# Kernel optimization log

Measured on AMD Instinct MI355X. Metric: run time of the kernel, lower is better.

## Reference

```python
import jax, jax.numpy as jnp
import numpy as np

N = 50000
E = 800000
NFEAT = 128
NHID = 128


def _glorot(key, shape):
    fan = shape[0] + shape[-1]
    s = jnp.sqrt(6.0 / fan)
    return jax.random.uniform(key, shape, jnp.float32, -s, s)


def setup_inputs() -> dict:
    key = jax.random.key(0)
    ks = jax.random.split(key, 8)
    x = jax.random.normal(ks[0], (N, NFEAT), jnp.float32)
    edge_index = jax.random.randint(ks[1], (2, E), 0, N, jnp.int64)
    return {
        "x": x,
        "edge_index": edge_index,
        "Wl1": _glorot(ks[2], (NFEAT, NHID)),
        "bl1": jnp.zeros((NHID,), jnp.float32),
        "Wr1": _glorot(ks[3], (NFEAT, NHID)),
        "br1": jnp.zeros((NHID,), jnp.float32),
        "att1": _glorot(ks[4], (NHID,)),
        "b1": jnp.zeros((NHID,), jnp.float32),
        "Wl2": _glorot(ks[5], (NHID, NHID)),
        "bl2": jnp.zeros((NHID,), jnp.float32),
        "Wr2": _glorot(ks[6], (NHID, NHID)),
        "br2": jnp.zeros((NHID,), jnp.float32),
        "att2": _glorot(ks[7], (NHID,)),
        "b2": jnp.zeros((NHID,), jnp.float32),
    }


def gatv2_conv(x, src, dst, Wl, bl, Wr, br, att, bias, neg_slope=0.2):
    # PyG GATv2Conv, heads=1, concat=True, add_self_loops handled by caller.
    xl = x @ Wl + bl                      # [N, H] source transform
    xr = x @ Wr + br                      # [N, H] target transform
    e = jax.nn.leaky_relu(xl[src] + xr[dst], neg_slope) @ att  # [E']
    # segment softmax over incoming edges per destination node
    m = jax.ops.segment_max(e, dst, num_segments=x.shape[0])
    w = jnp.exp(e - m[dst])
    denom = jax.ops.segment_sum(w, dst, num_segments=x.shape[0])
    alpha = w / denom[dst]                # [E']
    out = jax.ops.segment_sum(alpha[:, None] * xl[src], dst,
                              num_segments=x.shape[0])
    return out + bias


def reference(x, edge_index, Wl1, bl1, Wr1, br1, att1, b1,
              Wl2, bl2, Wr2, br2, att2, b2):
    n = x.shape[0]
    loop = jnp.arange(n, dtype=edge_index.dtype)
    src = jnp.concatenate([edge_index[0], loop])  # add self loops (PyG default)
    dst = jnp.concatenate([edge_index[1], loop])
    h = gatv2_conv(x, src, dst, Wl1, bl1, Wr1, br1, att1, b1)
    h = jax.nn.leaky_relu(h, 0.01)  # F.leaky_relu default slope
    out = gatv2_conv(h, src, dst, Wl2, bl2, Wr2, br2, att2, b2)
    return out
```

## Files before the change

### kernel.cpp

```cpp
#include <hip/hip_runtime.h>
#include <math.h>

#define HD 128
#define CHUNK 2048
#define MAXBINS 512
#define NPB 128
#define CAP 3072

typedef __attribute__((ext_vector_type(8))) short bf16x8;
typedef __attribute__((ext_vector_type(4))) float f32x4;

__device__ __forceinline__ unsigned short f2bf(float f) {
    unsigned int u = __float_as_uint(f);
    u += 0x7FFFu + ((u >> 16) & 1u);
    return (unsigned short)(u >> 16);
}
__device__ __forceinline__ float bflo(unsigned int p) {
    return __uint_as_float(p << 16);
}
__device__ __forceinline__ float bfhi(unsigned int p) {
    return __uint_as_float(p & 0xFFFF0000u);
}

__global__ __launch_bounds__(256) void wprep_kernel(
    const float* __restrict__ W0, const float* __restrict__ W1,
    const float* __restrict__ W2, const float* __restrict__ W3,
    uint4* __restrict__ T0, uint4* __restrict__ T1,
    uint4* __restrict__ T2, uint4* __restrict__ T3)
{
    const int m = blockIdx.x >> 3;
    const int s = (blockIdx.x & 7) * 256 + threadIdx.x;
    const float* W = (m == 0) ? W0 : (m == 1) ? W1 : (m == 2) ? W2 : W3;
    uint4* T = (m == 0) ? T0 : (m == 1) ? T1 : (m == 2) ? T2 : T3;

    const int l = s & 63;
    const int ckk = s >> 6;
    const int kk = ckk & 3;
    const int c = ckk >> 2;
    const int k0 = kk * 32 + (l >> 4) * 8;
    const int col = c * 16 + (l & 15);

    unsigned int b[8];
    #pragma unroll
    for (int j = 0; j < 8; ++j)
        b[j] = f2bf(W[(size_t)(k0 + j) * HD + col]);
    uint4 o;
    o.x = b[0] | (b[1] << 16);
    o.y = b[2] | (b[3] << 16);
    o.z = b[4] | (b[5] << 16);
    o.w = b[6] | (b[7] << 16);
    T[s] = o;
}

__global__ __launch_bounds__(256, 3) void gemm_mfma_kernel(
    const float* __restrict__ X,
    const uint4* __restrict__ WlF, const float* __restrict__ bl,
    const uint4* __restrict__ WrF, const float* __restrict__ br,
    unsigned short* __restrict__ Ylb, float* __restrict__ Yr, int n)
{
    __shared__ unsigned short xs[64 * HD];
    __shared__ uint4 bs[2048];
    const int row0 = blockIdx.x * 64;
    const int tid = threadIdx.x;
    const int lane = tid & 63;
    const int wv = tid >> 6;

    {
        const float4* Xv = (const float4*)(X + (size_t)row0 * HD);
        #pragma unroll
        for (int i = 0; i < 8; ++i) {
            int idx = tid + i * 256;
            int row = idx >> 5;
            int c4 = idx & 31;
            float4 v = make_float4(0.f, 0.f, 0.f, 0.f);
            if (row0 + row < n) v = Xv[idx];
            ushort4 b;
            b.x = f2bf(v.x); b.y = f2bf(v.y); b.z = f2bf(v.z); b.w = f2bf(v.w);
            int byteoff = row * 256 + ((c4 * 8) ^ ((row & 7) << 4));
            *(ushort4*)((char*)xs + byteoff) = b;
        }
    }
    #pragma unroll
    for (int i = 0; i < 8; ++i) bs[tid + i * 256] = WlF[tid + i * 256];
    __syncthreads();

    const int r15 = lane & 15;
    const int kg = lane >> 4;
    const int arow = wv * 16 + r15;
    const int abase = arow * 256;
    const int aswz = (arow & 7) << 4;

    bf16x8 af[4];
    #pragma unroll
    for (int kk = 0; kk < 4; ++kk)
        af[kk] = *(const bf16x8*)((const char*)xs + abase + ((kk * 64 + kg * 16) ^ aswz));

    const int orow0 = row0 + wv * 16 + kg * 4;

    {
        f32x4 acc[8];
        #pragma unroll
        for (int i = 0; i < 8; ++i) acc[i] = (f32x4){0.f, 0.f, 0.f, 0.f};
        #pragma unroll
        for (int kk = 0; kk < 4; ++kk) {
            #pragma unroll
            for (int c = 0; c < 8; ++c) {
                bf16x8 bf = *(const bf16x8*)&bs[(c * 4 + kk) * 64 + lane];
                acc[c] = __builtin_amdgcn_mfma_f32_16x16x32_bf16(af[kk], bf, acc[c], 0, 0, 0);
            }
        }
        __syncthreads();
        #pragma unroll
        for (int c = 0; c < 8; ++c) {
            const int col = c * 16 + r15;
            const float bLv = bl[col];
            #pragma unroll
            for (int r = 0; r < 4; ++r) {
                int row = orow0 + r;
                if (row < n) Ylb[(size_t)row * HD + col] = f2bf(acc[c][r] + bLv);
            }
        }
    }

    #pragma unroll
    for (int i = 0; i < 8; ++i) bs[tid + i * 256] = WrF[tid + i * 256];
    __syncthreads();

    {
        f32x4 acc[8];
        #pragma unroll
        for (int i = 0; i < 8; ++i) acc[i] = (f32x4){0.f, 0.f, 0.f, 0.f};
        #pragma unroll
        for (int kk = 0; kk < 4; ++kk) {
            #pragma unroll
            for (int c = 0; c < 8; ++c) {
                bf16x8 bf = *(const bf16x8*)&bs[(c * 4 + kk) * 64 + lane];
                acc[c] = __builtin_amdgcn_mfma_f32_16x16x32_bf16(af[kk], bf, acc[c], 0, 0, 0);
            }
        }
        #pragma unroll
        for (int c = 0; c < 8; ++c) {
            const int col = c * 16 + r15;
            const float bRv = br[col];
            #pragma unroll
            for (int r = 0; r < 4; ++r) {
                int row = orow0 + r;
                if (row < n) Yr[(size_t)row * HD + col] = acc[c][r] + bRv;
            }
        }
    }
}

__global__ __launch_bounds__(512) void cursor_init_kernel(int* __restrict__ binCursor, int nbins)
{
    int b = blockIdx.x * blockDim.x + threadIdx.x;
    if (b < nbins) binCursor[b] = b * CAP;
}

__global__ __launch_bounds__(256) void bin_scatter_kernel(
    const int* __restrict__ ei, int* __restrict__ binCursor,
    unsigned int* __restrict__ binned, int nE, int nTot, int nbins)
{
    __shared__ int hist[MAXBINS];
    __shared__ int base[MAXBINS];
    for (int i = threadIdx.x; i < nbins; i += 256) hist[i] = 0;
    __syncthreads();
    const int e0 = blockIdx.x * CHUNK;
    const int e1 = min(e0 + CHUNK, nTot);
    for (int e = e0 + threadIdx.x; e < e1; e += 256) {
        int d = (e < nE) ? ei[nE + e] : (e - nE);
        atomicAdd(&hist[d >> 7], 1);
    }
    __syncthreads();
    for (int b = threadIdx.x; b < nbins; b += 256) {
        int c = hist[b];
        base[b] = c ? atomicAdd(&binCursor[b], c) : 0;
        hist[b] = 0;
    }
    __syncthreads();
    for (int e = e0 + threadIdx.x; e < e1; e += 256) {
        int s, d;
        if (e < nE) { s = ei[e]; d = ei[nE + e]; }
        else        { s = e - nE; d = s; }
        int b = d >> 7;
        int r = atomicAdd(&hist[b], 1);
        binned[base[b] + r] = (unsigned int)s | ((unsigned int)(d & (NPB - 1)) << 16);
    }
}

__global__ __launch_bounds__(256) void bin_csr_kernel(
    const int* __restrict__ binCursor, const unsigned int* __restrict__ binned,
    int* __restrict__ rowstart, int* __restrict__ rowlen,
    int* __restrict__ csr_src, int n)
{
    __shared__ int hist[NPB];
    __shared__ int cur[NPB];
    __shared__ int sm[256];
    const int b = blockIdx.x;
    const int tid = threadIdx.x;
    const int lo = b * CAP;
    const int hi = binCursor[b];

    if (tid < NPB) hist[tid] = 0;
    __syncthreads();
    for (int e = lo + tid; e < hi; e += 256)
        atomicAdd(&hist[(binned[e] >> 16) & (NPB - 1)], 1);
    __syncthreads();
    const int c = (tid < NPB) ? hist[tid] : 0;
    const int rl = (c + 3) & ~3;
    sm[tid] = rl;
    __syncthreads();
    #pragma unroll
    for (int off = 1; off < 256; off <<= 1) {
        int v = (tid >= off) ? sm[tid - off] : 0;
        __syncthreads();
        sm[tid] += v;
        __syncthreads();
    }
    const int excl = sm[tid] - rl;
    if (tid < NPB) {
        cur[tid] = excl;
        int node = b * NPB + tid;
        if (node < n) { rowstart[node] = lo + excl; rowlen[node] = c; }
    }
    __syncthreads();
    for (int e = lo + tid; e < hi; e += 256) {
        unsigned int p = binned[e];
        int r = atomicAdd(&cur[(p >> 16) & (NPB - 1)], 1);
        csr_src[lo + r] = (int)(p & 0xFFFFu);
    }
    __syncthreads();
    if (tid < NPB) {
        int node = b * NPB + tid;
        if (node < n) {
            for (int r2 = excl + c; r2 < excl + rl; ++r2) csr_src[lo + r2] = node;
        }
    }
    int total = sm[255];
    if (tid < 64) csr_src[lo + total + tid] = 0;
}

__device__ __forceinline__ void gat4(
    uint2 u0, uint2 u1, uint2 u2, uint2 u3,
    const float4 xrv, const float4 attv, int k0, int len,
    float& den, float4& acc)
{
    float4 c0 = make_float4(bflo(u0.x), bfhi(u0.x), bflo(u0.y), bfhi(u0.y));
    float4 c1 = make_float4(bflo(u1.x), bfhi(u1.x), bflo(u1.y), bfhi(u1.y));
    float4 c2 = make_float4(bflo(u2.x), bfhi(u2.x), bflo(u2.y), bfhi(u2.y));
    float4 c3 = make_float4(bflo(u3.x), bfhi(u3.x), bflo(u3.y), bfhi(u3.y));

    float t0, t1, t2, t3;
    {
        float v;
        t0 = 0.f;
        v = c0.x + xrv.x; v = fmaxf(v, 0.2f * v); t0 = fmaf(v, attv.x, t0);
        v = c0.y + xrv.y; v = fmaxf(v, 0.2f * v); t0 = fmaf(v, attv.y, t0);
        v = c0.z + xrv.z; v = fmaxf(v, 0.2f * v); t0 = fmaf(v, attv.z, t0);
        v = c0.w + xrv.w; v = fmaxf(v, 0.2f * v); t0 = fmaf(v, attv.w, t0);
        t1 = 0.f;
        v = c1.x + xrv.x; v = fmaxf(v, 0.2f * v); t1 = fmaf(v, attv.x, t1);
        v = c1.y + xrv.y; v = fmaxf(v, 0.2f * v); t1 = fmaf(v, attv.y, t1);
        v = c1.z + xrv.z; v = fmaxf(v, 0.2f * v); t1 = fmaf(v, attv.z, t1);
        v = c1.w + xrv.w; v = fmaxf(v, 0.2f * v); t1 = fmaf(v, attv.w, t1);
        t2 = 0.f;
        v = c2.x + xrv.x; v = fmaxf(v, 0.2f * v); t2 = fmaf(v, attv.x, t2);
        v = c2.y + xrv.y; v = fmaxf(v, 0.2f * v); t2 = fmaf(v, attv.y, t2);
        v = c2.z + xrv.z; v = fmaxf(v, 0.2f * v); t2 = fmaf(v, attv.z, t2);
        v = c2.w + xrv.w; v = fmaxf(v, 0.2f * v); t2 = fmaf(v, attv.w, t2);
        t3 = 0.f;
        v = c3.x + xrv.x; v = fmaxf(v, 0.2f * v); t3 = fmaf(v, attv.x, t3);
        v = c3.y + xrv.y; v = fmaxf(v, 0.2f * v); t3 = fmaf(v, attv.y, t3);
        v = c3.z + xrv.z; v = fmaxf(v, 0.2f * v); t3 = fmaf(v, attv.z, t3);
        v = c3.w + xrv.w; v = fmaxf(v, 0.2f * v); t3 = fmaf(v, attv.w, t3);
    }

    #pragma unroll
    for (int off = 16; off >= 1; off >>= 1) {
        t0 += __shfl_xor(t0, off);
        t1 += __shfl_xor(t1, off);
        t2 += __shfl_xor(t2, off);
        t3 += __shfl_xor(t3, off);
    }

    if (k0 + 0 >= len) t0 = -1e30f;
    if (k0 + 1 >= len) t1 = -1e30f;
    if (k0 + 2 >= len) t2 = -1e30f;
    if (k0 + 3 >= len) t3 = -1e30f;

    float p0 = __expf(t0);
    float p1 = __expf(t1);
    float p2 = __expf(t2);
    float p3 = __expf(t3);
    den += (p0 + p1) + (p2 + p3);
    acc.x += (p0 * c0.x + p1 * c1.x) + (p2 * c2.x + p3 * c3.x);
    acc.y += (p0 * c0.y + p1 * c1.y) + (p2 * c2.y + p3 * c3.y);
    acc.z += (p0 * c0.z + p1 * c1.z) + (p2 * c2.z + p3 * c3.z);
    acc.w += (p0 * c0.w + p1 * c1.w) + (p2 * c2.w + p3 * c3.w);
}

__global__ __launch_bounds__(256) void fused_gat_kernel(
    const int* __restrict__ rowstart, const int* __restrict__ rowlen,
    const int* __restrict__ csr_src,
    const unsigned short* __restrict__ xlb, const float* __restrict__ xr,
    const float* __restrict__ att, const float* __restrict__ bias,
    float* __restrict__ out, int n, int doAct)
{
    const int wid  = blockIdx.x * 4 + (threadIdx.x >> 6);
    const int lane = threadIdx.x & 63;
    const int d    = wid * 2 + (lane >> 5);
    const int fl   = (lane & 31) * 4;

    const float4 attv = *(const float4*)(att + fl);
    float4 xrv = make_float4(0.f, 0.f, 0.f, 0.f);
    int rp = 0, len = 0;
    if (d < n) {
        xrv = *(const float4*)(xr + (size_t)d * HD + fl);
        rp  = rowstart[d];
        len = rowlen[d];
    }
    const int rl = (len + 3) & ~3;
    const int ml = max(rl, __shfl_xor(rl, 32));

    float den = 0.f;
    float4 acc = make_float4(0.f, 0.f, 0.f, 0.f);

    const unsigned short* xfl = xlb + fl;

    uint2 a0, a1, a2, a3, b0, b1, b2, b3;
    {
        int i0 = csr_src[rp + 0], i1 = csr_src[rp + 1];
        int i2 = csr_src[rp + 2], i3 = csr_src[rp + 3];
        int j0 = csr_src[rp + 4], j1 = csr_src[rp + 5];
        int j2 = csr_src[rp + 6], j3 = csr_src[rp + 7];
        a0 = *(const uint2*)(xfl + (size_t)i0 * HD);
        a1 = *(const uint2*)(xfl + (size_t)i1 * HD);
        a2 = *(const uint2*)(xfl + (size_t)i2 * HD);
        a3 = *(const uint2*)(xfl + (size_t)i3 * HD);
        b0 = *(const uint2*)(xfl + (size_t)j0 * HD);
        b1 = *(const uint2*)(xfl + (size_t)j1 * HD);
        b2 = *(const uint2*)(xfl + (size_t)j2 * HD);
        b3 = *(const uint2*)(xfl + (size_t)j3 * HD);
    }

    for (int k0 = 0; k0 < ml; k0 += 8) {
        uint2 u0 = a0, u1 = a1, u2 = a2, u3 = a3;
        int kn = k0 + 8;
        if (kn < ml) {
            int i0 = csr_src[rp + kn + 0], i1 = csr_src[rp + kn + 1];
            int i2 = csr_src[rp + kn + 2], i3 = csr_src[rp + kn + 3];
            a0 = *(const uint2*)(xfl + (size_t)i0 * HD);
            a1 = *(const uint2*)(xfl + (size_t)i1 * HD);
            a2 = *(const uint2*)(xfl + (size_t)i2 * HD);
            a3 = *(const uint2*)(xfl + (size_t)i3 * HD);
        }
        gat4(u0, u1, u2, u3, xrv, attv, k0, len, den, acc);

        if (k0 + 4 < ml) {
            uint2 v0 = b0, v1 = b1, v2 = b2, v3 = b3;
            int km = k0 + 12;
            if (km < ml) {
                int j0 = csr_src[rp + km + 0], j1 = csr_src[rp + km + 1];
                int j2 = csr_src[rp + km + 2], j3 = csr_src[rp + km + 3];
                b0 = *(const uint2*)(xfl + (size_t)j0 * HD);
                b1 = *(const uint2*)(xfl + (size_t)j1 * HD);
                b2 = *(const uint2*)(xfl + (size_t)j2 * HD);
                b3 = *(const uint2*)(xfl + (size_t)j3 * HD);
            }
            gat4(v0, v1, v2, v3, xrv, attv, k0 + 4, len, den, acc);
        }
    }

    if (d < n) {
        const float4 bv = *(const float4*)(bias + fl);
        float inv = 1.f / den;
        float o0 = acc.x * inv + bv.x;
        float o1 = acc.y * inv + bv.y;
        float o2 = acc.z * inv + bv.z;
        float o3 = acc.w * inv + bv.w;
        if (doAct) {
            o0 = (o0 > 0.f) ? o0 : 0.01f * o0;
            o1 = (o1 > 0.f) ? o1 : 0.01f * o1;
            o2 = (o2 > 0.f) ? o2 : 0.01f * o2;
            o3 = (o3 > 0.f) ? o3 : 0.01f * o3;
        }
        *(float4*)(out + (size_t)d * HD + fl) = make_float4(o0, o1, o2, o3);
    }
}

extern "C" void kernel_launch(void* const* d_in, const int* in_sizes, int n_in,
                              void* d_out, int out_size, void* d_ws, size_t ws_size,
                              hipStream_t stream)
{
    const float* x    = (const float*)d_in[0];
    const int*   ei   = (const int*)d_in[1];
    const float* Wl1  = (const float*)d_in[2];
    const float* bl1  = (const float*)d_in[3];
    const float* Wr1  = (const float*)d_in[4];
    const float* br1  = (const float*)d_in[5];
    const float* att1 = (const float*)d_in[6];
    const float* b1   = (const float*)d_in[7];
    const float* Wl2  = (const float*)d_in[8];
    const float* bl2  = (const float*)d_in[9];
    const float* Wr2  = (const float*)d_in[10];
    const float* br2  = (const float*)d_in[11];
    const float* att2 = (const float*)d_in[12];
    const float* b2   = (const float*)d_in[13];

    const int n    = in_sizes[0] / HD;
    const int E    = in_sizes[1] / 2;
    const int nTot = E + n;
    const int nbins = (n + NPB - 1) / NPB;

    char* ws = (char*)d_ws;
    const size_t feat_bytes = (size_t)n * HD * sizeof(float);
    const size_t bf_bytes   = ((size_t)n * HD * 2 + 511) & ~(size_t)511;
    const size_t wt_bytes   = ((size_t)HD * HD * 2 + 511) & ~(size_t)511;
    auto alignup = [](size_t v) { return (v + 511) & ~(size_t)511; };
    unsigned short* xlb = (unsigned short*)ws; ws += bf_bytes;
    float* xr = (float*)ws;          ws += feat_bytes;
    float* h  = (float*)ws;          ws += feat_bytes;
    uint4* wlF1 = (uint4*)ws; ws += wt_bytes;
    uint4* wrF1 = (uint4*)ws; ws += wt_bytes;
    uint4* wlF2 = (uint4*)ws; ws += wt_bytes;
    uint4* wrF2 = (uint4*)ws; ws += wt_bytes;
    int* binCursor = (int*)ws;       ws += alignup((size_t)nbins * 4);
    int* rowstart  = (int*)ws;       ws += alignup((size_t)n * 4);
    int* rowlen    = (int*)ws;       ws += alignup((size_t)n * 4);
    unsigned int* binned = (unsigned int*)ws; ws += alignup((size_t)nbins * CAP * 4);
    int* csr_src   = (int*)ws;       ws += alignup((size_t)nbins * CAP * 4);

    float* out = (float*)d_out;

    const int nChunk = (nTot + CHUNK - 1) / CHUNK;
    dim3 gb(256); dim3 gg((n + 63) / 64);
    dim3 fb(256); dim3 fg((n + 7) / 8);

    wprep_kernel<<<32, 256, 0, stream>>>(Wl1, Wr1, Wl2, Wr2, wlF1, wrF1, wlF2, wrF2);
    cursor_init_kernel<<<(nbins + 511) / 512, 512, 0, stream>>>(binCursor, nbins);
    bin_scatter_kernel<<<nChunk, 256, 0, stream>>>(ei, binCursor, binned, E, nTot, nbins);
    bin_csr_kernel<<<nbins, 256, 0, stream>>>(binCursor, binned, rowstart, rowlen, csr_src, n);

    gemm_mfma_kernel<<<gg, gb, 0, stream>>>(x, wlF1, bl1, wrF1, br1, xlb, xr, n);
    fused_gat_kernel<<<fg, fb, 0, stream>>>(rowstart, rowlen, csr_src, xlb, xr, att1, b1, h, n, 1);

    gemm_mfma_kernel<<<gg, gb, 0, stream>>>(h, wlF2, bl2, wrF2, br2, xlb, xr, n);
    fused_gat_kernel<<<fg, fb, 0, stream>>>(rowstart, rowlen, csr_src, xlb, xr, att2, b2, out, n, 0);
}
```

Measured before the change: 184.2 us.

## Degree-sort node pairs, store xr in bf16, prescale CSR offsets, preload Wr

Within each 128-node bin, a bitonic sort orders nodes by padded degree, and the GAT kernel maps half-wave pairs through this permutation so the two destinations sharing a wave have similar edge counts. The xr target transform is now stored as bf16 to halve its write and read traffic. CSR source indices are stored pre-shifted as byte offsets, which removes the multiply from the gather address. Wr weights are loaded into registers early so the load overlaps with the Wl GEMM. The trade-offs are lower precision for xr, a sort added to the CSR build, and scattered output rows.

```diff
diff --git a/kernel.cpp b/kernel.cpp
--- a/kernel.cpp
+++ b/kernel.cpp
@@ -56,7 +56,7 @@
     const float* __restrict__ X,
     const uint4* __restrict__ WlF, const float* __restrict__ bl,
     const uint4* __restrict__ WrF, const float* __restrict__ br,
-    unsigned short* __restrict__ Ylb, float* __restrict__ Yr, int n)
+    unsigned short* __restrict__ Ylb, unsigned short* __restrict__ Yrb, int n)
 {
     __shared__ unsigned short xs[64 * HD];
     __shared__ uint4 bs[2048];
@@ -64,6 +64,10 @@
     const int tid = threadIdx.x;
     const int lane = tid & 63;
     const int wv = tid >> 6;
+
+    uint4 wr_reg[8];
+    #pragma unroll
+    for (int i = 0; i < 8; ++i) wr_reg[i] = WrF[tid + i * 256];
 
     {
         const float4* Xv = (const float4*)(X + (size_t)row0 * HD);
@@ -123,7 +127,7 @@
     }
 
     #pragma unroll
-    for (int i = 0; i < 8; ++i) bs[tid + i * 256] = WrF[tid + i * 256];
+    for (int i = 0; i < 8; ++i) bs[tid + i * 256] = wr_reg[i];
     __syncthreads();
 
     {
@@ -145,7 +149,7 @@
             #pragma unroll
             for (int r = 0; r < 4; ++r) {
                 int row = orow0 + r;
-                if (row < n) Yr[(size_t)row * HD + col] = acc[c][r] + bRv;
+                if (row < n) Yrb[(size_t)row * HD + col] = f2bf(acc[c][r] + bRv);
             }
         }
     }
@@ -191,11 +195,12 @@
 __global__ __launch_bounds__(256) void bin_csr_kernel(
     const int* __restrict__ binCursor, const unsigned int* __restrict__ binned,
     int* __restrict__ rowstart, int* __restrict__ rowlen,
-    int* __restrict__ csr_src, int n)
+    int* __restrict__ csr_src, int* __restrict__ pairs, int n)
 {
     __shared__ int hist[NPB];
     __shared__ int cur[NPB];
     __shared__ int sm[256];
+    __shared__ unsigned int srt[NPB];
     const int b = blockIdx.x;
     const int tid = threadIdx.x;
     const int lo = b * CAP;
@@ -209,6 +214,7 @@
     const int c = (tid < NPB) ? hist[tid] : 0;
     const int rl = (c + 3) & ~3;
     sm[tid] = rl;
+    if (tid < NPB) srt[tid] = ((unsigned int)rl << 7) | (unsigned int)tid;
     __syncthreads();
     #pragma unroll
     for (int off = 1; off < 256; off <<= 1) {
@@ -224,16 +230,30 @@
         if (node < n) { rowstart[node] = lo + excl; rowlen[node] = c; }
     }
     __syncthreads();
+    for (int k = 2; k <= NPB; k <<= 1) {
+        for (int j = k >> 1; j > 0; j >>= 1) {
+            if (tid < NPB) {
+                int ixj = tid ^ j;
+                if (ixj > tid) {
+                    unsigned int a = srt[tid], bb = srt[ixj];
+                    bool asc = ((tid & k) == 0);
+                    if (asc ? (a > bb) : (a < bb)) { srt[tid] = bb; srt[ixj] = a; }
+                }
+            }
+            __syncthreads();
+        }
+    }
+    if (tid < NPB) pairs[b * NPB + tid] = b * NPB + (int)(srt[tid] & 127u);
     for (int e = lo + tid; e < hi; e += 256) {
         unsigned int p = binned[e];
         int r = atomicAdd(&cur[(p >> 16) & (NPB - 1)], 1);
-        csr_src[lo + r] = (int)(p & 0xFFFFu);
+        csr_src[lo + r] = (int)((p & 0xFFFFu) << 8);
     }
     __syncthreads();
     if (tid < NPB) {
         int node = b * NPB + tid;
         if (node < n) {
-            for (int r2 = excl + c; r2 < excl + rl; ++r2) csr_src[lo + r2] = node;
+            for (int r2 = excl + c; r2 < excl + rl; ++r2) csr_src[lo + r2] = node << 8;
         }
     }
     int total = sm[255];
@@ -300,22 +320,25 @@
 }
 
 __global__ __launch_bounds__(256) void fused_gat_kernel(
+    const int* __restrict__ pairs,
     const int* __restrict__ rowstart, const int* __restrict__ rowlen,
     const int* __restrict__ csr_src,
-    const unsigned short* __restrict__ xlb, const float* __restrict__ xr,
+    const unsigned short* __restrict__ xlb, const unsigned short* __restrict__ xrb,
     const float* __restrict__ att, const float* __restrict__ bias,
     float* __restrict__ out, int n, int doAct)
 {
     const int wid  = blockIdx.x * 4 + (threadIdx.x >> 6);
     const int lane = threadIdx.x & 63;
-    const int d    = wid * 2 + (lane >> 5);
+    const int dp   = wid * 2 + (lane >> 5);
+    const int d    = pairs[dp];
     const int fl   = (lane & 31) * 4;
 
     const float4 attv = *(const float4*)(att + fl);
     float4 xrv = make_float4(0.f, 0.f, 0.f, 0.f);
     int rp = 0, len = 0;
     if (d < n) {
-        xrv = *(const float4*)(xr + (size_t)d * HD + fl);
+        uint2 xru = *(const uint2*)(xrb + (size_t)d * HD + fl);
+        xrv = make_float4(bflo(xru.x), bfhi(xru.x), bflo(xru.y), bfhi(xru.y));
         rp  = rowstart[d];
         len = rowlen[d];
     }
@@ -325,34 +348,34 @@
     float den = 0.f;
     float4 acc = make_float4(0.f, 0.f, 0.f, 0.f);
 
-    const unsigned short* xfl = xlb + fl;
+    const char* xbase = (const char*)(xlb + fl);
 
     uint2 a0, a1, a2, a3, b0, b1, b2, b3;
     {
-        int i0 = csr_src[rp + 0], i1 = csr_src[rp + 1];
-        int i2 = csr_src[rp + 2], i3 = csr_src[rp + 3];
-        int j0 = csr_src[rp + 4], j1 = csr_src[rp + 5];
-        int j2 = csr_src[rp + 6], j3 = csr_src[rp + 7];
-        a0 = *(const uint2*)(xfl + (size_t)i0 * HD);
-        a1 = *(const uint2*)(xfl + (size_t)i1 * HD);
-        a2 = *(const uint2*)(xfl + (size_t)i2 * HD);
-        a3 = *(const uint2*)(xfl + (size_t)i3 * HD);
-        b0 = *(const uint2*)(xfl + (size_t)j0 * HD);
-        b1 = *(const uint2*)(xfl + (size_t)j1 * HD);
-        b2 = *(const uint2*)(xfl + (size_t)j2 * HD);
-        b3 = *(const uint2*)(xfl + (size_t)j3 * HD);
+        int o0 = csr_src[rp + 0], o1 = csr_src[rp + 1];
+        int o2 = csr_src[rp + 2], o3 = csr_src[rp + 3];
+        int q0 = csr_src[rp + 4], q1 = csr_src[rp + 5];
+        int q2 = csr_src[rp + 6], q3 = csr_src[rp + 7];
+        a0 = *(const uint2*)(xbase + (size_t)(unsigned)o0);
+        a1 = *(const uint2*)(xbase + (size_t)(unsigned)o1);
+        a2 = *(const uint2*)(xbase + (size_t)(unsigned)o2);
+        a3 = *(const uint2*)(xbase + (size_t)(unsigned)o3);
+        b0 = *(const uint2*)(xbase + (size_t)(unsigned)q0);
+        b1 = *(const uint2*)(xbase + (size_t)(unsigned)q1);
+        b2 = *(const uint2*)(xbase + (size_t)(unsigned)q2);
+        b3 = *(const uint2*)(xbase + (size_t)(unsigned)q3);
     }
 
     for (int k0 = 0; k0 < ml; k0 += 8) {
         uint2 u0 = a0, u1 = a1, u2 = a2, u3 = a3;
         int kn = k0 + 8;
         if (kn < ml) {
-            int i0 = csr_src[rp + kn + 0], i1 = csr_src[rp + kn + 1];
-            int i2 = csr_src[rp + kn + 2], i3 = csr_src[rp + kn + 3];
-            a0 = *(const uint2*)(xfl + (size_t)i0 * HD);
-            a1 = *(const uint2*)(xfl + (size_t)i1 * HD);
-            a2 = *(const uint2*)(xfl + (size_t)i2 * HD);
-            a3 = *(const uint2*)(xfl + (size_t)i3 * HD);
+            int o0 = csr_src[rp + kn + 0], o1 = csr_src[rp + kn + 1];
+            int o2 = csr_src[rp + kn + 2], o3 = csr_src[rp + kn + 3];
+            a0 = *(const uint2*)(xbase + (size_t)(unsigned)o0);
+            a1 = *(const uint2*)(xbase + (size_t)(unsigned)o1);
+            a2 = *(const uint2*)(xbase + (size_t)(unsigned)o2);
+            a3 = *(const uint2*)(xbase + (size_t)(unsigned)o3);
         }
         gat4(u0, u1, u2, u3, xrv, attv, k0, len, den, acc);
 
@@ -360,12 +383,12 @@
             uint2 v0 = b0, v1 = b1, v2 = b2, v3 = b3;
             int km = k0 + 12;
             if (km < ml) {
-                int j0 = csr_src[rp + km + 0], j1 = csr_src[rp + km + 1];
-                int j2 = csr_src[rp + km + 2], j3 = csr_src[rp + km + 3];
-                b0 = *(const uint2*)(xfl + (size_t)j0 * HD);
-                b1 = *(const uint2*)(xfl + (size_t)j1 * HD);
-                b2 = *(const uint2*)(xfl + (size_t)j2 * HD);
-                b3 = *(const uint2*)(xfl + (size_t)j3 * HD);
+                int q0 = csr_src[rp + km + 0], q1 = csr_src[rp + km + 1];
+                int q2 = csr_src[rp + km + 2], q3 = csr_src[rp + km + 3];
+                b0 = *(const uint2*)(xbase + (size_t)(unsigned)q0);
+                b1 = *(const uint2*)(xbase + (size_t)(unsigned)q1);
+                b2 = *(const uint2*)(xbase + (size_t)(unsigned)q2);
+                b3 = *(const uint2*)(xbase + (size_t)(unsigned)q3);
             }
             gat4(v0, v1, v2, v3, xrv, attv, k0 + 4, len, den, acc);
         }
@@ -411,6 +434,7 @@
     const int E    = in_sizes[1] / 2;
     const int nTot = E + n;
     const int nbins = (n + NPB - 1) / NPB;
+    const int np   = nbins * NPB;
 
     char* ws = (char*)d_ws;
     const size_t feat_bytes = (size_t)n * HD * sizeof(float);
@@ -418,7 +442,7 @@
     const size_t wt_bytes   = ((size_t)HD * HD * 2 + 511) & ~(size_t)511;
     auto alignup = [](size_t v) { return (v + 511) & ~(size_t)511; };
     unsigned short* xlb = (unsigned short*)ws; ws += bf_bytes;
-    float* xr = (float*)ws;          ws += feat_bytes;
+    unsigned short* xrb = (unsigned short*)ws; ws += bf_bytes;
     float* h  = (float*)ws;          ws += feat_bytes;
     uint4* wlF1 = (uint4*)ws; ws += wt_bytes;
     uint4* wrF1 = (uint4*)ws; ws += wt_bytes;
@@ -427,6 +451,7 @@
     int* binCursor = (int*)ws;       ws += alignup((size_t)nbins * 4);
     int* rowstart  = (int*)ws;       ws += alignup((size_t)n * 4);
     int* rowlen    = (int*)ws;       ws += alignup((size_t)n * 4);
+    int* pairs     = (int*)ws;       ws += alignup((size_t)np * 4);
     unsigned int* binned = (unsigned int*)ws; ws += alignup((size_t)nbins * CAP * 4);
     int* csr_src   = (int*)ws;       ws += alignup((size_t)nbins * CAP * 4);
 
@@ -434,16 +459,16 @@
 
     const int nChunk = (nTot + CHUNK - 1) / CHUNK;
     dim3 gb(256); dim3 gg((n + 63) / 64);
-    dim3 fb(256); dim3 fg((n + 7) / 8);
+    dim3 fb(256); dim3 fg((np + 7) / 8);
 
     wprep_kernel<<<32, 256, 0, stream>>>(Wl1, Wr1, Wl2, Wr2, wlF1, wrF1, wlF2, wrF2);
     cursor_init_kernel<<<(nbins + 511) / 512, 512, 0, stream>>>(binCursor, nbins);
     bin_scatter_kernel<<<nChunk, 256, 0, stream>>>(ei, binCursor, binned, E, nTot, nbins);
-    bin_csr_kernel<<<nbins, 256, 0, stream>>>(binCursor, binned, rowstart, rowlen, csr_src, n);
-
-    gemm_mfma_kernel<<<gg, gb, 0, stream>>>(x, wlF1, bl1, wrF1, br1, xlb, xr, n);
-    fused_gat_kernel<<<fg, fb, 0, stream>>>(rowstart, rowlen, csr_src, xlb, xr, att1, b1, h, n, 1);
-
-    gemm_mfma_kernel<<<gg, gb, 0, stream>>>(h, wlF2, bl2, wrF2, br2, xlb, xr, n);
-    fused_gat_kernel<<<fg, fb, 0, stream>>>(rowstart, rowlen, csr_src, xlb, xr, att2, b2, out, n, 0);
-}
+    bin_csr_kernel<<<nbins, 256, 0, stream>>>(binCursor, binned, rowstart, rowlen, csr_src, pairs, n);
+
+    gemm_mfma_kernel<<<gg, gb, 0, stream>>>(x, wlF1, bl1, wrF1, br1, xlb, xrb, n);
+    fused_gat_kernel<<<fg, fb, 0, stream>>>(pairs, rowstart, rowlen, csr_src, xlb, xrb, att1, b1, h, n, 1);
+
+    gemm_mfma_kernel<<<gg, gb, 0, stream>>>(h, wlF2, bl2, wrF2, br2, xlb, xrb, n);
+    fused_gat_kernel<<<fg, fb, 0, stream>>>(pairs, rowstart, rowlen, csr_src, xlb, xrb, att2, b2, out, n, 0);
+}
```

Result: slower. 215.3 us (+16.9%).
